# Performance work log

Measured on AMD Instinct MI355X. Metric: run time of the kernel, lower is better.

## Reference

```python
import jax, jax.numpy as jnp
import numpy as np

DEPTH, HEADS, DIM_HEAD = 6, 8, 32
D_MODEL, D_FF = 256, 1024
B, N, D_IN, N_CLS = 4, 4096, 128, 10
NB_FEAT = int(DIM_HEAD * np.log(DIM_HEAD))  # 110 random features (performer_pytorch default)


def _ortho_gaussian(m, d, rng):
    # gaussian orthogonal random projection (FAVOR+), rows rescaled by chi-distributed norms
    blocks = []
    for _ in range(int(np.ceil(m / d))):
        q, _ = np.linalg.qr(rng.standard_normal((d, d)))
        blocks.append(q.T)
    mat = np.concatenate(blocks, 0)[:m]
    mult = np.linalg.norm(rng.standard_normal((m, d)), axis=1)
    return (mult[:, None] * mat).astype(np.float32)


def setup_inputs() -> dict:
    rng = np.random.default_rng(0)
    w = lambda *s: jnp.asarray((rng.standard_normal(s) * 0.02).astype(np.float32))
    z = lambda *s: jnp.zeros(s, jnp.float32)
    o = lambda *s: jnp.ones(s, jnp.float32)
    proj = jnp.asarray(np.stack([_ortho_gaussian(NB_FEAT, DIM_HEAD, rng) for _ in range(DEPTH)]))
    return dict(
        x=jnp.asarray(rng.standard_normal((B, N, D_IN)).astype(np.float32)),
        mask=jnp.ones((B, N), bool),
        w_in=w(D_IN, D_MODEL), b_in=z(D_MODEL),
        ln1_g=o(DEPTH, D_MODEL), ln1_b=z(DEPTH, D_MODEL),
        wq=w(DEPTH, D_MODEL, D_MODEL), wk=w(DEPTH, D_MODEL, D_MODEL),
        wv=w(DEPTH, D_MODEL, D_MODEL), wo=w(DEPTH, D_MODEL, D_MODEL), bo=z(DEPTH, D_MODEL),
        proj=proj,
        ln2_g=o(DEPTH, D_MODEL), ln2_b=z(DEPTH, D_MODEL),
        w1=w(DEPTH, D_MODEL, D_FF), b1=z(DEPTH, D_FF),
        w2=w(DEPTH, D_FF, D_MODEL), b2=z(DEPTH, D_MODEL),
        cls_g=o(D_MODEL), cls_b=z(D_MODEL),
        wc1=w(D_MODEL, D_MODEL), bc1=z(D_MODEL),
        wc2=w(D_MODEL, N_CLS), bc2=z(N_CLS),
    )


def _ln(x, g, b, eps=1e-5):
    mu = x.mean(-1, keepdims=True)
    var = ((x - mu) ** 2).mean(-1, keepdims=True)
    return (x - mu) * jax.lax.rsqrt(var + eps) * g + b


def _softmax_kernel(data, proj, is_query, eps=1e-4):
    # FAVOR+ positive softmax features (performer_pytorch softmax_kernel)
    dn = data.shape[-1] ** -0.25
    ratio = proj.shape[0] ** -0.5
    dd = jnp.einsum('bhnd,md->bhnm', data * dn, proj)
    diag = 0.5 * (dn ** 2) * jnp.sum(data ** 2, axis=-1, keepdims=True)  # [B,H,N,1]
    if is_query:
        m = jnp.max(dd, axis=-1, keepdims=True)
    else:
        m = jnp.max(dd, axis=(-2, -1), keepdims=True)
    m = jax.lax.stop_gradient(m)
    return ratio * (jnp.exp(dd - diag - m) + eps)


def _linear_attn(q, k, v):
    # non-causal O(n) attention: q,k [B,H,N,M], v [B,H,N,dh]
    k_sum = k.sum(-2)                                            # [B,H,M]
    d_inv = 1.0 / jnp.einsum('bhnm,bhm->bhn', q, k_sum)          # [B,H,N]
    ctx = jnp.einsum('bhnm,bhnd->bhmd', k, v)                    # [B,H,M,dh]
    return jnp.einsum('bhnm,bhmd,bhn->bhnd', q, ctx, d_inv)


def _forward(x, mask, w_in, b_in, ln1_g, ln1_b, wq, wk, wv, wo, bo, proj,
             ln2_g, ln2_b, w1, b1, w2, b2, cls_g, cls_b, wc1, bc1, wc2, bc2):
    b_, n_ = x.shape[:2]
    h = x @ w_in + b_in
    mb = mask[:, None, :, None]
    split = lambda t: t.reshape(b_, n_, HEADS, DIM_HEAD).transpose(0, 2, 1, 3)
    for i in range(DEPTH):
        y = _ln(h, ln1_g[i], ln1_b[i])
        q, k, v = split(y @ wq[i]), split(y @ wk[i]), split(y @ wv[i])
        v = jnp.where(mb, v, 0.0)
        qp = _softmax_kernel(q, proj[i], True)
        kp = _softmax_kernel(k, proj[i], False)
        a = _linear_attn(qp, kp, v).transpose(0, 2, 1, 3).reshape(b_, n_, D_MODEL)
        h = h + a @ wo[i] + bo[i]
        y2 = _ln(h, ln2_g[i], ln2_b[i])
        h = h + jax.nn.gelu(y2 @ w1[i] + b1[i], approximate=False) @ w2[i] + b2[i]
    p = h.mean(1)
    z = jax.nn.relu(_ln(p, cls_g, cls_b))
    z = jax.nn.relu(z @ wc1 + bc1)
    return z @ wc2 + bc2


def reference(x, mask, w_in, b_in, ln1_g, ln1_b, wq, wk, wv, wo, bo, proj,
              ln2_g, ln2_b, w1, b1, w2, b2, cls_g, cls_b, wc1, bc1, wc2, bc2):
    return _forward(x, mask, w_in, b_in, ln1_g, ln1_b, wq, wk, wv, wo, bo, proj,
                    ln2_g, ln2_b, w1, b1, w2, b2, cls_g, cls_b, wc1, bc1, wc2, bc2)
```

## Files before the change

### kernel.cpp

```cpp
#include <hip/hip_runtime.h>
#include <cstdint>
#include <cstddef>

typedef __attribute__((ext_vector_type(8))) short bf16x8;
typedef __attribute__((ext_vector_type(4))) float f32x4;
typedef unsigned short u16;
typedef unsigned int u32;

static constexpr float DN    = 0.42044820762685725f;
static constexpr float DN2   = 0.17677669529663687f;
static constexpr float RATIO = 0.09534625892455924f;
static constexpr float KEPS  = 1e-4f;

__device__ __forceinline__ float b2f(u16 u) {
    union { float f; u32 i; } x; x.i = ((u32)u) << 16; return x.f;
}
__device__ __forceinline__ u16 f2b(float f) {
    union { float f; u32 i; } x; x.f = f;
    u32 r = (x.i + 0x7FFFu + ((x.i >> 16) & 1u)) >> 16;
    return (u16)r;
}
__device__ __forceinline__ float wred_sum(float v) {
#pragma unroll
    for (int o = 32; o > 0; o >>= 1) v += __shfl_xor(v, o, 64);
    return v;
}
__device__ __forceinline__ float gelu_f(float v) {
    return 0.5f * v * (1.f + erff(v * 0.7071067811865475f));
}
__device__ __forceinline__ void gload16(const u16* g, u16* l) {
    __builtin_amdgcn_global_load_lds(
        (const __attribute__((address_space(1))) u32*)(const u32*)g,
        (__attribute__((address_space(3))) u32*)(u32*)l, 16, 0, 0);
}

__global__ __launch_bounds__(256) void trk(const float* __restrict__ src, u16* __restrict__ dst,
                                           int K, int N)
{
    const size_t bo = (size_t)blockIdx.z * K * N;
    src += bo; dst += bo;
    __shared__ float tl[32][33];
    const int t = threadIdx.x, tx = t & 31, ty = t >> 5;
    const int k0 = blockIdx.y * 32, n0 = blockIdx.x * 32;
#pragma unroll
    for (int p = 0; p < 4; ++p)
        tl[ty + p * 8][tx] = src[(size_t)(k0 + ty + p * 8) * N + n0 + tx];
    __syncthreads();
#pragma unroll
    for (int p = 0; p < 4; ++p)
        dst[(size_t)(n0 + ty + p * 8) * K + k0 + tx] = f2b(tl[tx][ty + p * 8]);
}

__global__ __launch_bounds__(256) void trkf(const float* __restrict__ src, float* __restrict__ dst,
                                            int K, int N)
{
    __shared__ float tl[32][33];
    const int t = threadIdx.x, tx = t & 31, ty = t >> 5;
    const int k0 = blockIdx.y * 32, n0 = blockIdx.x * 32;
#pragma unroll
    for (int p = 0; p < 4; ++p)
        tl[ty + p * 8][tx] = src[(size_t)(k0 + ty + p * 8) * N + n0 + tx];
    __syncthreads();
#pragma unroll
    for (int p = 0; p < 4; ++p)
        dst[(size_t)(n0 + ty + p * 8) * K + k0 + tx] = tl[tx][ty + p * 8];
}

__global__ __launch_bounds__(256) void xcast(const float* __restrict__ x, u16* __restrict__ xb)
{
    const int i = blockIdx.x * 256 + threadIdx.x;
    const float4 v = ((const float4*)x)[i];
    uint2 r;
    r.x = (u32)f2b(v.x) | ((u32)f2b(v.y) << 16);
    r.y = (u32)f2b(v.z) | ((u32)f2b(v.w) << 16);
    ((uint2*)xb)[i] = r;
}

template<int CMODE, int NP, bool QKV, bool AHEAD, bool CHEAD, bool CHUNK, int DEPTH>
__global__ __launch_bounds__(512) void gemm3(
    const u16* __restrict__ A, const u16* __restrict__ Bt,
    const float* __restrict__ bias, u16* __restrict__ Cb, int ldc,
    u16* __restrict__ hres, const float* __restrict__ lng, const float* __restrict__ lnb,
    u16* __restrict__ yout, int K, int lda, int nrt)
{
    constexpr int KC    = (NP == 128) ? 256 : 128;
    constexpr int SLOTS = KC / 8;
    constexpr int SSH   = (SLOTS == 32) ? 5 : 4;
    constexpr int BB    = NP * KC * 2;
    constexpr int ABYT  = 64 * KC * 2;
    constexpr int NCB   = NP / 128;
    constexpr int CTS   = (NP == 128) ? 136 : 264;
    constexpr int EPI   = (CMODE <= 1) ? (64 * CTS * 2) : (64 * 264 * 2 + 4608);
    constexpr int KCC   = 64;
    constexpr int BBC   = 256 * KCC * 2;
    constexpr int ABYTC = 64 * KCC * 2;
    constexpr int BUF   = BBC + ABYTC;
    constexpr int LDSZ  = CHUNK ? (DEPTH * BUF) : (BB + 2 * ABYT + EPI);
    __shared__ __align__(16) char smem[LDSZ];

    const u16* Btl = Bt;
    u16* Cbl = Cb;
    if (QKV) { Btl += (size_t)blockIdx.z * 393216; Cbl += (size_t)blockIdx.z * 4194304; }
    const int t = threadIdx.x, w = t >> 6, lr = (t & 63) & 15, lg = (t & 63) >> 4;
    const int p = blockIdx.x;

    char* epi = CHUNK ? smem : (smem + BB + 2 * ABYT);

    f32x4 acc[4][NCB];
    auto ZERO = [&]() {
#pragma unroll
        for (int i = 0; i < 4; ++i)
#pragma unroll
            for (int j = 0; j < NCB; ++j) acc[i][j] = f32x4{0.f, 0.f, 0.f, 0.f};
    };

    auto EPILOGUE = [&](int row0) {
        if constexpr (CMODE <= 1) {
            u16* ctile = (u16*)epi;
            float bv[NCB];
#pragma unroll
            for (int cb = 0; cb < NCB; ++cb) {
                const int col = p * NP + w * (NP / 8) + cb * 16 + lr;
                bv[cb] = bias ? bias[col] : 0.f;
            }
#pragma unroll
            for (int rbk = 0; rbk < 4; ++rbk)
#pragma unroll
                for (int cb = 0; cb < NCB; ++cb)
#pragma unroll
                    for (int rr = 0; rr < 4; ++rr) {
                        const int rl = rbk * 16 + 4 * lg + rr;
                        float v = acc[rbk][cb][rr] + bv[cb];
                        if (CMODE == 1) v = gelu_f(v);
                        ctile[rl * CTS + w * (NP / 8) + cb * 16 + lr] = f2b(v);
                    }
            __syncthreads();
            if constexpr (CHEAD && NP == 128) {
                const int bq = row0 >> 12, n0 = row0 & 4095;
#pragma unroll
                for (int i = 0; i < 2; ++i) {
                    const int u = i * 512 + t;
                    const int hh = u >> 8, rem = u & 255;
                    const int row = rem >> 2, dblk = rem & 3;
                    *(uint4*)(Cbl + ((size_t)(bq * 8 + p * 4 + hh) * 4096 + n0 + row) * 32 + dblk * 8)
                        = *(const uint4*)&ctile[row * CTS + hh * 32 + dblk * 8];
                }
            } else if constexpr (CHEAD && NP == 256) {
                const int bq = row0 >> 12, n0 = row0 & 4095;
#pragma unroll
                for (int i = 0; i < 4; ++i) {
                    const int u = i * 512 + t;
                    const int row = u >> 5, seg = u & 31;
                    const int hh = seg >> 2, dblk = seg & 3;
                    *(uint4*)(Cbl + ((size_t)(bq * 8 + hh) * 4096 + n0 + row) * 32 + dblk * 8)
                        = *(const uint4*)&ctile[row * 264 + seg * 8];
                }
            } else {
                constexpr int NIT = (NP == 128) ? 2 : 4;
                constexpr int SEGM = NP / 8 - 1;
                constexpr int RSH = (NP == 128) ? 4 : 5;
#pragma unroll
                for (int i = 0; i < NIT; ++i) {
                    const int u = i * 512 + t;
                    const int row = u >> RSH, seg = u & SEGM;
                    *(uint4*)(Cbl + (size_t)(row0 + row) * ldc + p * NP + seg * 8)
                        = *(const uint4*)&ctile[row * CTS + seg * 8];
                }
            }
        } else {
            u16*   ctile = (u16*)epi;
            float* rsum  = (float*)(epi + 33792);
            float* rsum2 = rsum + 512;
            float* rmu   = rsum2 + 512;
            float* rrs   = rmu + 64;
            int cidx[NCB]; float bv[NCB];
#pragma unroll
            for (int cb = 0; cb < NCB; ++cb) {
                cidx[cb] = w * 32 + cb * 16 + lr;
                bv[cb] = bias ? bias[cidx[cb]] : 0.f;
            }
            if constexpr (CMODE == 2 || CMODE == 4) {
#pragma unroll
                for (int i = 0; i < 4; ++i) {
                    const int u = i * 512 + t;
                    const int row = u >> 5, seg = u & 31;
                    *(uint4*)&ctile[row * 264 + seg * 8]
                        = *(const uint4*)(hres + (size_t)(row0 + row) * 256 + seg * 8);
                }
                __syncthreads();
            }
#pragma unroll
            for (int rbk = 0; rbk < 4; ++rbk)
#pragma unroll
                for (int cb = 0; cb < NCB; ++cb)
#pragma unroll
                    for (int rr = 0; rr < 4; ++rr) {
                        const int rl = rbk * 16 + 4 * lg + rr;
                        float v = acc[rbk][cb][rr] + bv[cb];
                        if constexpr (CMODE == 2 || CMODE == 4)
                            v += b2f(ctile[rl * 264 + cidx[cb]]);
                        acc[rbk][cb][rr] = v;
                    }
            __syncthreads();
            if constexpr (CMODE != 4) {
#pragma unroll
                for (int rbk = 0; rbk < 4; ++rbk)
#pragma unroll
                    for (int rr = 0; rr < 4; ++rr) {
                        float s1 = acc[rbk][0][rr] + acc[rbk][NCB - 1][rr];
                        float s2 = fmaf(acc[rbk][0][rr], acc[rbk][0][rr],
                                        acc[rbk][NCB - 1][rr] * acc[rbk][NCB - 1][rr]);
#pragma unroll
                        for (int off = 1; off < 16; off <<= 1) {
                            s1 += __shfl_xor(s1, off, 64);
                            s2 += __shfl_xor(s2, off, 64);
                        }
                        if (lr == 0) {
                            const int rl = rbk * 16 + 4 * lg + rr;
                            rsum[rl * 8 + w] = s1; rsum2[rl * 8 + w] = s2;
                        }
                    }
                __syncthreads();
                if (t < 64) {
                    float s1 = 0.f, s2 = 0.f;
#pragma unroll
                    for (int j = 0; j < 8; ++j) { s1 += rsum[t * 8 + j]; s2 += rsum2[t * 8 + j]; }
                    const float mu = s1 * (1.f / 256.f);
                    const float var = s2 * (1.f / 256.f) - mu * mu;
                    rmu[t] = mu; rrs[t] = rsqrtf(var + 1e-5f);
                }
                __syncthreads();
            }
#pragma unroll
            for (int rbk = 0; rbk < 4; ++rbk)
#pragma unroll
                for (int cb = 0; cb < NCB; ++cb)
#pragma unroll
                    for (int rr = 0; rr < 4; ++rr) {
                        const int rl = rbk * 16 + 4 * lg + rr;
                        ctile[rl * 264 + cidx[cb]] = f2b(acc[rbk][cb][rr]);
                    }
            __syncthreads();
#pragma unroll
            for (int i = 0; i < 4; ++i) {
                const int u = i * 512 + t;
                const int row = u >> 5, seg = u & 31;
                *(uint4*)(hres + (size_t)(row0 + row) * 256 + seg * 8)
                    = *(const uint4*)&ctile[row * 264 + seg * 8];
            }
            if constexpr (CMODE != 4) {
                __syncthreads();
                float gv[NCB], bb2[NCB];
#pragma unroll
                for (int cb = 0; cb < NCB; ++cb) { gv[cb] = lng[cidx[cb]]; bb2[cb] = lnb[cidx[cb]]; }
#pragma unroll
                for (int rbk = 0; rbk < 4; ++rbk)
#pragma unroll
                    for (int cb = 0; cb < NCB; ++cb)
#pragma unroll
                        for (int rr = 0; rr < 4; ++rr) {
                            const int rl = rbk * 16 + 4 * lg + rr;
                            const float yv = (acc[rbk][cb][rr] - rmu[rl]) * rrs[rl] * gv[cb] + bb2[cb];
                            ctile[rl * 264 + cidx[cb]] = f2b(yv);
                        }
                __syncthreads();
#pragma unroll
                for (int i = 0; i < 4; ++i) {
                    const int u = i * 512 + t;
                    const int row = u >> 5, seg = u & 31;
                    *(uint4*)(yout + (size_t)(row0 + row) * 256 + seg * 8)
                        = *(const uint4*)&ctile[row * 264 + seg * 8];
                }
            }
        }
    };

    if constexpr (!CHUNK) {
        u16* Bs  = (u16*)smem;
        u16* Asm = (u16*)(smem + BB);
        auto STAGE_B = [&](int c) {
#pragma unroll
            for (int i = 0; i < BB / 16 / 512; ++i) {
                const int u = i * 512 + t;
                const int col = u >> SSH, slot = u & (SLOTS - 1);
                const int gs = slot ^ (col & 7);
                gload16(Btl + (size_t)(p * NP + col) * K + c * KC + gs * 8, Bs + u * 8);
            }
        };
        auto STAGE_A = [&](int c, int row0, int buf) {
            u16* dst = Asm + buf * (ABYT / 2);
#pragma unroll
            for (int i = 0; i < ABYT / 16 / 512; ++i) {
                const int u = i * 512 + t;
                const int row = u >> SSH, slot = u & (SLOTS - 1);
                const int gs = slot ^ (row & 7);
                const u16* src;
                if (AHEAD) {
                    const int kg = c * KC + gs * 8;
                    src = A + ((size_t)((row0 >> 12) * 8 + (kg >> 5)) * 4096 + (row0 & 4095) + row) * 32 + (kg & 31);
                } else {
                    src = A + (size_t)(row0 + row) * lda + c * KC + gs * 8;
                }
                gload16(src, dst + u * 8);
            }
        };
        auto KLOOP = [&](const u16* AcC) {
#pragma unroll
            for (int ks = 0; ks < KC / 32; ++ks) {
                bf16x8 af[4], bfv[NCB];
#pragma unroll
                for (int rbk = 0; rbk < 4; ++rbk) {
                    const int row = rbk * 16 + lr;
                    af[rbk] = *(const bf16x8*)&AcC[row * KC + (((ks * 4 + lg) ^ (row & 7)) << 3)];
                }
#pragma unroll
                for (int cb = 0; cb < NCB; ++cb) {
                    const int col = w * (NP / 8) + cb * 16 + lr;
                    bfv[cb] = *(const bf16x8*)&Bs[col * KC + (((ks * 4 + lg) ^ (col & 7)) << 3)];
                }
#pragma unroll
                for (int rbk = 0; rbk < 4; ++rbk)
#pragma unroll
                    for (int cb = 0; cb < NCB; ++cb)
                        acc[rbk][cb] = __builtin_amdgcn_mfma_f32_16x16x32_bf16(af[rbk], bfv[cb], acc[rbk][cb], 0, 0, 0);
            }
        };
        int ab = 0;
        STAGE_B(0);
        STAGE_A(0, blockIdx.y * nrt * 64, 0);
        asm volatile("s_waitcnt vmcnt(0)" ::: "memory");
        __syncthreads();
        for (int rt = 0; rt < nrt; ++rt) {
            const int row0 = (blockIdx.y * nrt + rt) * 64;
            if (rt + 1 < nrt) STAGE_A(0, row0 + 64, ab ^ 1);
            ZERO();
            KLOOP(Asm + ab * (ABYT / 2));
            EPILOGUE(row0);
            asm volatile("s_waitcnt vmcnt(0)" ::: "memory");
            __syncthreads();
            ab ^= 1;
        }
    } else {
        const int NC = K / KCC;
        const int row0 = blockIdx.y * 64;
        auto STAGE_CH = [&](int c, int b) {
            u16* bsB = (u16*)(smem + b * BUF);
            u16* bsA = (u16*)(smem + b * BUF + BBC);
#pragma unroll
            for (int i = 0; i < BBC / 16 / 512; ++i) {
                const int u = i * 512 + t;
                const int col = u >> 3, slot = u & 7;
                const int gs = slot ^ (col & 7);
                gload16(Btl + (size_t)(p * NP + col) * K + c * KCC + gs * 8, bsB + u * 8);
            }
            {
                const int u = t;
                const int row = u >> 3, slot = u & 7;
                const int gs = slot ^ (row & 7);
                const u16* src;
                if (AHEAD) {
                    const int kg = c * KCC + gs * 8;
                    src = A + ((size_t)((row0 >> 12) * 8 + (kg >> 5)) * 4096 + (row0 & 4095) + row) * 32 + (kg & 31);
                } else {
                    src = A + (size_t)(row0 + row) * lda + c * KCC + gs * 8;
                }
                gload16(src, bsA + u * 8);
            }
        };
        auto KLOOP_C = [&](const u16* BsC, const u16* AcC) {
#pragma unroll
            for (int ks = 0; ks < 2; ++ks) {
                bf16x8 af[4], bfv[NCB];
#pragma unroll
                for (int rbk = 0; rbk < 4; ++rbk) {
                    const int row = rbk * 16 + lr;
                    af[rbk] = *(const bf16x8*)&AcC[row * KCC + (((ks * 4 + lg) ^ (row & 7)) << 3)];
                }
#pragma unroll
                for (int cb = 0; cb < NCB; ++cb) {
                    const int col = w * 32 + cb * 16 + lr;
                    bfv[cb] = *(const bf16x8*)&BsC[col * KCC + (((ks * 4 + lg) ^ (col & 7)) << 3)];
                }
#pragma unroll
                for (int rbk = 0; rbk < 4; ++rbk)
#pragma unroll
                    for (int cb = 0; cb < NCB; ++cb)
                        acc[rbk][cb] = __builtin_amdgcn_mfma_f32_16x16x32_bf16(af[rbk], bfv[cb], acc[rbk][cb], 0, 0, 0);
            }
        };

        ZERO();
#pragma unroll
        for (int d = 0; d < DEPTH; ++d)
            if (d < NC) STAGE_CH(d, d);
        for (int c = 0; c < NC; ++c) {
            const int rem = NC - 1 - c;
            if constexpr (DEPTH == 3) {
                if (rem >= 2)      asm volatile("s_waitcnt vmcnt(10)" ::: "memory");
                else if (rem == 1) asm volatile("s_waitcnt vmcnt(5)"  ::: "memory");
                else               asm volatile("s_waitcnt vmcnt(0)"  ::: "memory");
            } else {
                if (rem >= 1)      asm volatile("s_waitcnt vmcnt(5)"  ::: "memory");
                else               asm volatile("s_waitcnt vmcnt(0)"  ::: "memory");
            }
            __builtin_amdgcn_s_barrier();
            __builtin_amdgcn_sched_barrier(0);
            const int cb_ = c % DEPTH;
            KLOOP_C((const u16*)(smem + cb_ * BUF),
                    (const u16*)(smem + cb_ * BUF + BBC));
            __builtin_amdgcn_sched_barrier(0);
            if (c + DEPTH < NC) {
                __builtin_amdgcn_s_barrier();
                __builtin_amdgcn_sched_barrier(0);
                STAGE_CH(c + DEPTH, cb_);
            }
        }
        __builtin_amdgcn_s_barrier();
        __builtin_amdgcn_sched_barrier(0);
        EPILOGUE(row0);
    }
}

__global__ __launch_bounds__(256) void kctx2(
    const u16* __restrict__ kg, const u16* __restrict__ vg,
    const float* __restrict__ proj, float* __restrict__ ctxp, float* __restrict__ Mcp,
    float* __restrict__ vsump)
{
    __shared__ __align__(16) u16 projS[112 * 32];
    __shared__ __align__(16) u16 kS[128 * 32];
    __shared__ __align__(16) u16 vTS[48 * 128];
    __shared__ __align__(16) u16 eTS[112 * 128];
    __shared__ float diagS[128];
    __shared__ float redS[4];
    const int t = threadIdx.x, w = t >> 6, lane = t & 63, lr = lane & 15, lg = lane >> 4;
    const int bh = blockIdx.x >> 3, chunk = blockIdx.x & 7;

    for (int idx = t; idx < 112 * 32; idx += 256) {
        const int m = idx >> 5, d = idx & 31;
        projS[idx] = (m < 110) ? f2b(proj[m * 32 + d] * DN) : (u16)0;
    }
    for (int idx = t; idx < 16 * 128; idx += 256) {
        const int rr = idx >> 7;
        vTS[(32 + rr) * 128 + (idx & 127)] = (rr == 0) ? f2b(1.0f) : (u16)0;
    }
    for (int idx = t; idx < 16 * 128; idx += 256)
        eTS[112 * 128 + idx] = 0;

    f32x4 E[2][3];
#pragma unroll
    for (int i = 0; i < 2; ++i)
#pragma unroll
        for (int j = 0; j < 3; ++j) E[i][j] = f32x4{0.f, 0.f, 0.f, 0.f};
    float Mrun = -INFINITY;
    float vsAcc = 0.f;

    for (int r = 0; r < 4; ++r) {
        const size_t eb = ((size_t)bh * 4096 + chunk * 512 + r * 128) * 32;
#pragma unroll
        for (int i = 0; i < 2; ++i) {
            const int u = i * 256 + t;
            ((uint4*)kS)[u] = ((const uint4*)(kg + eb))[u];
        }
#pragma unroll
        for (int i = 0; i < 2; ++i) {
            const int u = i * 256 + t;
            const int tok = u >> 2, dblk = u & 3;
            union { uint4 v; u16 s[8]; } uu;
            uu.v = ((const uint4*)(vg + eb))[u];
#pragma unroll
            for (int j = 0; j < 8; ++j) {
                const int d = dblk * 8 + j;
                vTS[d * 128 + ((((tok >> 3) ^ (d & 15))) << 3) + (tok & 7)] = uu.s[j];
            }
        }
        __syncthreads();
        {
            const int d = t >> 3, seg = t & 7;
            union { uint4 v; u16 s[8]; } ua, ub;
            ua.v = *(const uint4*)&vTS[d * 128 + seg * 16];
            ub.v = *(const uint4*)&vTS[d * 128 + seg * 16 + 8];
            float s = 0.f;
#pragma unroll
            for (int j = 0; j < 8; ++j) s += b2f(ua.s[j]) + b2f(ub.s[j]);
            vsAcc += s;
        }
        if (t < 128) {
            float s = 0.f;
#pragma unroll
            for (int dq = 0; dq < 4; ++dq) {
                union { uint4 v; u16 ss[8]; } uu;
                uu.v = ((const uint4*)kS)[t * 4 + dq];
#pragma unroll
                for (int j = 0; j < 8; ++j) { const float f = b2f(uu.ss[j]); s = fmaf(f, f, s); }
            }
            diagS[t] = 0.5f * DN2 * s;
        }
        __syncthreads();
        f32x4 dd[7][2];
#pragma unroll
        for (int mb = 0; mb < 7; ++mb)
#pragma unroll
            for (int tb = 0; tb < 2; ++tb) dd[mb][tb] = f32x4{0.f, 0.f, 0.f, 0.f};
        bf16x8 kf[2];
#pragma unroll
        for (int tb = 0; tb < 2; ++tb)
            kf[tb] = *(const bf16x8*)&kS[(w * 32 + tb * 16 + lr) * 32 + lg * 8];
#pragma unroll
        for (int mb = 0; mb < 7; ++mb) {
            const bf16x8 pf = *(const bf16x8*)&projS[(mb * 16 + lr) * 32 + lg * 8];
#pragma unroll
            for (int tb = 0; tb < 2; ++tb)
                dd[mb][tb] = __builtin_amdgcn_mfma_f32_16x16x32_bf16(pf, kf[tb], dd[mb][tb], 0, 0, 0);
        }
        float mx = -INFINITY;
#pragma unroll
        for (int mb = 0; mb < 7; ++mb)
#pragma unroll
            for (int tb = 0; tb < 2; ++tb)
#pragma unroll
                for (int rr = 0; rr < 4; ++rr) {
                    if (mb == 6 && (4 * lg + rr) >= 14) continue;
                    mx = fmaxf(mx, dd[mb][tb][rr]);
                }
#pragma unroll
        for (int off = 1; off < 64; off <<= 1) mx = fmaxf(mx, __shfl_xor(mx, off, 64));
        if (lane == 0) redS[w] = mx;
        __syncthreads();
        float Mnew = fmaxf(fmaxf(redS[0], redS[1]), fmaxf(redS[2], redS[3]));
        Mnew = fmaxf(Mrun, Mnew);
        const float scl = __expf(Mrun - Mnew);
#pragma unroll
        for (int i = 0; i < 2; ++i)
#pragma unroll
            for (int j = 0; j < 3; ++j)
#pragma unroll
                for (int rr = 0; rr < 4; ++rr) E[i][j][rr] *= scl;
        Mrun = Mnew;
        const float dg0 = diagS[w * 32 + lr], dg1 = diagS[w * 32 + 16 + lr];
#pragma unroll
        for (int mb = 0; mb < 7; ++mb)
#pragma unroll
            for (int tb = 0; tb < 2; ++tb)
#pragma unroll
                for (int rr = 0; rr < 4; ++rr) {
                    const int tok = w * 32 + tb * 16 + lr;
                    const int m = mb * 16 + 4 * lg + rr;
                    const float e = __expf(dd[mb][tb][rr] - (tb ? dg1 : dg0) - Mnew);
                    eTS[m * 128 + ((((tok >> 3) ^ (m & 15))) << 3) + (tok & 7)] = f2b(e);
                }
        __syncthreads();
#pragma unroll
        for (int ks = 0; ks < 4; ++ks) {
            bf16x8 aF[2], bF[3];
#pragma unroll
            for (int mb2 = 0; mb2 < 2; ++mb2) {
                const int m = w * 32 + mb2 * 16 + lr;
                aF[mb2] = *(const bf16x8*)&eTS[m * 128 + (((ks * 4 + lg) ^ lr) << 3)];
            }
#pragma unroll
            for (int nb = 0; nb < 3; ++nb) {
                const int d = nb * 16 + lr;
                bF[nb] = *(const bf16x8*)&vTS[d * 128 + (((ks * 4 + lg) ^ lr) << 3)];
            }
#pragma unroll
            for (int mb2 = 0; mb2 < 2; ++mb2)
#pragma unroll
                for (int nb = 0; nb < 3; ++nb)
                    E[mb2][nb] = __builtin_amdgcn_mfma_f32_16x16x32_bf16(aF[mb2], bF[nb], E[mb2][nb], 0, 0, 0);
        }
        __syncthreads();
    }
    const size_t ob = (size_t)blockIdx.x * 112 * 33;
// ... 162 lines not shown
    f32x4 o[2][2];
#pragma unroll
    for (int i = 0; i < 2; ++i)
#pragma unroll
        for (int j = 0; j < 2; ++j) o[i][j] = f32x4{0.f, 0.f, 0.f, 0.f};
#pragma unroll
    for (int ks = 0; ks < 4; ++ks) {
        bf16x8 aF[2], bF[2];
#pragma unroll
        for (int tb = 0; tb < 2; ++tb) {
            const int tok = w * 32 + tb * 16 + lr;
            aF[tb] = *(const bf16x8*)&pS[tok * 128 + (((ks * 4 + lg) ^ lr) << 3)];
        }
#pragma unroll
        for (int nb = 0; nb < 2; ++nb) {
            const int d = nb * 16 + lr;
            bF[nb] = *(const bf16x8*)&ctxTS[d * 128 + (((ks * 4 + lg) ^ lr) << 3)];
        }
#pragma unroll
        for (int tb = 0; tb < 2; ++tb)
#pragma unroll
            for (int nb = 0; nb < 2; ++nb)
                o[tb][nb] = __builtin_amdgcn_mfma_f32_16x16x32_bf16(aF[tb], bF[nb], o[tb][nb], 0, 0, 0);
    }
    u16* outS = qS;
#pragma unroll
    for (int tb = 0; tb < 2; ++tb)
#pragma unroll
        for (int nb = 0; nb < 2; ++nb)
#pragma unroll
            for (int rr = 0; rr < 4; ++rr) {
                const int tokl = w * 32 + tb * 16 + 4 * lg + rr;
                outS[tokl * 32 + nb * 16 + lr] = f2b(o[tb][nb][rr] * dinvS[tokl]);
            }
    __syncthreads();
#pragma unroll
    for (int i = 0; i < 2; ++i) {
        const int u = i * 256 + t;
        ((uint4*)(ag + qeb))[u] = ((const uint4*)outS)[u];
    }
}

__global__ __launch_bounds__(256) void pool_k(const u16* __restrict__ h,
                                              float* __restrict__ pp)
{
    const int b = blockIdx.x, ch = blockIdx.y, d = threadIdx.x;
    const u16* p = h + ((size_t)b * 4096 + ch * 256) * 256 + d;
    float s = 0.f;
    for (int n = 0; n < 256; ++n) s += b2f(p[(size_t)n * 256]);
    pp[(b * 16 + ch) * 256 + d] = s;
}

__global__ __launch_bounds__(256) void cls_a(const float* __restrict__ pp,
                                             const float* __restrict__ g,
                                             const float* __restrict__ bb,
                                             float* __restrict__ zA)
{
    const int b = blockIdx.x, t = threadIdx.x, w = t >> 6, lane = t & 63;
    __shared__ float red1[4], red2[4];
    float s = 0.f;
#pragma unroll
    for (int c = 0; c < 16; ++c) s += pp[(b * 16 + c) * 256 + t];
    const float p = s * (1.f / 4096.f);
    const float s1 = wred_sum(p);
    const float s2 = wred_sum(p * p);
    if (lane == 0) { red1[w] = s1; red2[w] = s2; }
    __syncthreads();
    const float S1 = red1[0] + red1[1] + red1[2] + red1[3];
    const float S2 = red2[0] + red2[1] + red2[2] + red2[3];
    const float mu = S1 * (1.f / 256.f);
    const float var = S2 * (1.f / 256.f) - mu * mu;
    const float rr = rsqrtf(var + 1e-5f);
    zA[b * 256 + t] = fmaxf((p - mu) * rr * g[t] + bb[t], 0.f);
}

__global__ __launch_bounds__(256) void cls_b(const float* __restrict__ zA,
                                             const float* __restrict__ wc1T,
                                             const float* __restrict__ bc1,
                                             float* __restrict__ zB)
{
    const int b = blockIdx.x, t = threadIdx.x;
    __shared__ float zS[256];
    zS[t] = zA[b * 256 + t];
    __syncthreads();
    float s = bc1[t];
    const float* wr = wc1T + (size_t)t * 256;
#pragma unroll
    for (int i = 0; i < 64; ++i) {
        const float4 v = ((const float4*)wr)[i];
        s = fmaf(zS[i * 4 + 0], v.x, s);
        s = fmaf(zS[i * 4 + 1], v.y, s);
        s = fmaf(zS[i * 4 + 2], v.z, s);
        s = fmaf(zS[i * 4 + 3], v.w, s);
    }
    zB[b * 256 + t] = fmaxf(s, 0.f);
}

__global__ __launch_bounds__(256) void cls_c(const float* __restrict__ zB,
                                             const float* __restrict__ wc2,
                                             const float* __restrict__ bc2,
                                             float* __restrict__ out)
{
    const int b = blockIdx.x, t = threadIdx.x, w = t >> 6, lane = t & 63;
    __shared__ float red[4][10];
    const float v = zB[b * 256 + t];
    float a[10];
#pragma unroll
    for (int c = 0; c < 10; ++c) a[c] = v * wc2[t * 10 + c];
#pragma unroll
    for (int c = 0; c < 10; ++c) {
        const float s = wred_sum(a[c]);
        if (lane == 0) red[w][c] = s;
    }
    __syncthreads();
    if (t < 10) out[b * 10 + t] = bc2[t] + red[0][t] + red[1][t] + red[2][t] + red[3][t];
}

extern "C" void kernel_launch(void* const* d_in, const int* in_sizes, int n_in,
                              void* d_out, int out_size, void* d_ws, size_t ws_size,
                              hipStream_t stream)
{
    const float* x    = (const float*)d_in[0];
    const float* w_in = (const float*)d_in[2];
    const float* b_in = (const float*)d_in[3];
    const float* ln1g = (const float*)d_in[4];
    const float* ln1b = (const float*)d_in[5];
    const float* wq   = (const float*)d_in[6];
    const float* wk   = (const float*)d_in[7];
    const float* wv   = (const float*)d_in[8];
    const float* wo   = (const float*)d_in[9];
    const float* bo   = (const float*)d_in[10];
    const float* proj = (const float*)d_in[11];
    const float* ln2g = (const float*)d_in[12];
    const float* ln2b = (const float*)d_in[13];
    const float* w1   = (const float*)d_in[14];
    const float* b1   = (const float*)d_in[15];
    const float* w2   = (const float*)d_in[16];
    const float* b2   = (const float*)d_in[17];
    const float* clsg = (const float*)d_in[18];
    const float* clsb = (const float*)d_in[19];
    const float* wc1  = (const float*)d_in[20];
    const float* bc1  = (const float*)d_in[21];
    const float* wc2  = (const float*)d_in[22];
    const float* bc2  = (const float*)d_in[23];

    char* wsb = (char*)d_ws;
    const size_t MB = 1024 * 1024;
    u16* h     = (u16*)(wsb);
    u16* y     = (u16*)(wsb + 16 * MB);
    u16* qb    = (u16*)(wsb + 24 * MB);
    u16* kb    = (u16*)(wsb + 32 * MB);
    u16* vb    = (u16*)(wsb + 40 * MB);
    u16* ab    = (u16*)(wsb + 48 * MB);
    u16* mid   = qb;
    u16* xb    = (u16*)(wsb + 56 * MB);
    u16* wtb   = (u16*)(wsb + 60 * MB);
    u16* w_inT = wtb;
    u16* wqT   = w_inT + 32768;
    u16* wkT   = wqT + 393216;
    u16* wvT   = wkT + 393216;
    u16* woT   = wvT + 393216;
    u16* w1T   = woT + 393216;
    u16* w2T   = w1T + 1572864;
    char* p2   = (char*)(w2T + 1572864);
    float* ctxp  = (float*)p2;
    float* Mcp   = ctxp + 256 * 112 * 33;
    u16*   ctxTg = (u16*)(Mcp + 256);
    float* ksumg = (float*)(ctxTg + 32 * 4096);
    float* pp    = ksumg + 32 * 128;
    float* vsump = pp + 16384;
    float* zA    = vsump + 8192;
    float* zB    = zA + 1024;
    float* wc1T  = zB + 1024;

    trk<<<dim3(8, 4, 1), 256, 0, stream>>>(w_in, w_inT, 128, 256);
    trk<<<dim3(8, 8, 6), 256, 0, stream>>>(wq, wqT, 256, 256);
    trk<<<dim3(8, 8, 6), 256, 0, stream>>>(wk, wkT, 256, 256);
    trk<<<dim3(8, 8, 6), 256, 0, stream>>>(wv, wvT, 256, 256);
    trk<<<dim3(8, 8, 6), 256, 0, stream>>>(wo, woT, 256, 256);
    trk<<<dim3(32, 8, 6), 256, 0, stream>>>(w1, w1T, 256, 1024);
    trk<<<dim3(8, 32, 6), 256, 0, stream>>>(w2, w2T, 1024, 256);
    trkf<<<dim3(8, 8, 1), 256, 0, stream>>>(wc1, wc1T, 256, 256);
    xcast<<<2048, 256, 0, stream>>>(x, xb);

    gemm3<3, 256, false, false, false, false, 2><<<dim3(1, 256), 512, 0, stream>>>(
        xb, w_inT, b_in, nullptr, 256, h, ln1g, ln1b, y, 128, 128, 1);
    for (int i = 0; i < 6; ++i) {
        const float* proj_i = proj + (size_t)i * 3520;
        gemm3<0, 256, true, false, true, true, 2><<<dim3(1, 256, 3), 512, 0, stream>>>(
            y, wqT + (size_t)i * 65536, nullptr, qb, 256,
            nullptr, nullptr, nullptr, nullptr, 256, 256, 1);
        kctx2<<<256, 256, 0, stream>>>(kb, vb, proj_i, ctxp, Mcp, vsump);
        kred2<<<32, 256, 0, stream>>>(ctxp, Mcp, vsump, ctxTg, ksumg);
        qattn2<<<1024, 256, 0, stream>>>(qb, proj_i, ctxTg, ksumg, ab);
        gemm3<2, 256, false, true, false, true, 3><<<dim3(1, 256), 512, 0, stream>>>(
            ab, woT + (size_t)i * 65536, bo + i * 256, nullptr, 256, h,
            ln2g + i * 256, ln2b + i * 256, y, 256, 0, 1);
        gemm3<1, 256, false, false, false, true, 2><<<dim3(4, 256), 512, 0, stream>>>(
            y, w1T + (size_t)i * 262144, b1 + i * 1024, mid, 1024,
            nullptr, nullptr, nullptr, nullptr, 256, 256, 1);
        if (i < 5)
            gemm3<2, 256, false, false, false, true, 3><<<dim3(1, 256), 512, 0, stream>>>(
                mid, w2T + (size_t)i * 262144, b2 + i * 256, nullptr, 256, h,
                ln1g + (i + 1) * 256, ln1b + (i + 1) * 256, y, 1024, 1024, 1);
        else
            gemm3<4, 256, false, false, false, true, 3><<<dim3(1, 256), 512, 0, stream>>>(
                mid, w2T + (size_t)i * 262144, b2 + i * 256, nullptr, 256, h,
                nullptr, nullptr, nullptr, 1024, 1024, 1);
    }
    pool_k<<<dim3(4, 16), 256, 0, stream>>>(h, pp);
    cls_a<<<4, 256, 0, stream>>>(pp, clsg, clsb, zA);
    cls_b<<<4, 256, 0, stream>>>(zA, wc1T, bc1, zB);
    cls_c<<<4, 256, 0, stream>>>(zB, wc2, bc2, (float*)d_out);
}
```

Baseline: 821.4 us.

## Fuse FFN up-projection, GELU and down-projection into one kernel

Replaces the separate W1 GEMM (writing a 1024-wide intermediate to global memory) and W2 GEMM with a single kernel per 64-row tile. The kernel computes 256-column chunks of the GELU intermediate into shared memory and immediately accumulates them into the W2 output, then applies bias, residual and the next LayerNorm. This removes the global write and read of the intermediate activation and one launch per layer. In exchange it uses 128KB of shared memory per block with only 256 blocks, which lowers occupancy and parallelism, and it reads y and writes y in place, which is safe only because each block stages its own rows first.

```diff
diff --git a/kernel.cpp b/kernel.cpp
--- a/kernel.cpp
+++ b/kernel.cpp
@@ -418,6 +418,238 @@
         __builtin_amdgcn_s_barrier();
         __builtin_amdgcn_sched_barrier(0);
         EPILOGUE(row0);
+    }
+}
+
+template<int CMODE2>
+__global__ __launch_bounds__(512) void ffuse(
+    const u16* __restrict__ yg, const u16* __restrict__ w1T, const float* __restrict__ b1,
+    const u16* __restrict__ w2T, const float* __restrict__ b2,
+    u16* __restrict__ hres, const float* __restrict__ lng, const float* __restrict__ lnb,
+    u16* __restrict__ yout)
+{
+    __shared__ __align__(16) char smem[131072];
+    u16* yS   = (u16*)smem;
+    u16* midS = (u16*)(smem + 32768);
+    u16* wb   = (u16*)(smem + 65536);
+    char* epi = smem + 65536;
+
+    const int t = threadIdx.x, w = t >> 6, lr = (t & 63) & 15, lg = (t & 63) >> 4;
+    const int row0 = blockIdx.x * 64;
+
+#pragma unroll
+    for (int i = 0; i < 4; ++i) {
+        const int u = i * 512 + t;
+        const int row = u >> 5, s32 = u & 31;
+        const int kc = s32 >> 3, sl = s32 & 7;
+        const int gs = sl ^ (row & 7);
+        gload16(yg + (size_t)(row0 + row) * 256 + kc * 64 + gs * 8, yS + u * 8);
+    }
+
+    auto STAGE_J = [&](int j, int b) {
+        const int mp = j >> 3, ph = (j >> 2) & 1, kc = j & 3;
+        u16* dst = wb + b * 16384;
+#pragma unroll
+        for (int i = 0; i < 4; ++i) {
+            const int u = i * 512 + t;
+            const int col = u >> 3, sl = u & 7;
+            const int gs = sl ^ (col & 7);
+            const u16* src = (ph == 0)
+                ? (w1T + (size_t)(mp * 256 + col) * 256 + kc * 64 + gs * 8)
+                : (w2T + (size_t)col * 1024 + mp * 256 + kc * 64 + gs * 8);
+            gload16(src, dst + u * 8);
+        }
+    };
+
+    f32x4 acc1[4][2], acc2[4][2];
+#pragma unroll
+    for (int i = 0; i < 4; ++i)
+#pragma unroll
+        for (int j = 0; j < 2; ++j) acc2[i][j] = f32x4{0.f, 0.f, 0.f, 0.f};
+
+    STAGE_J(0, 0);
+    STAGE_J(1, 1);
+
+#pragma unroll
+    for (int j = 0; j < 32; ++j) {
+        if (j < 31) asm volatile("s_waitcnt vmcnt(4)" ::: "memory");
+        else        asm volatile("s_waitcnt vmcnt(0)" ::: "memory");
+        __builtin_amdgcn_s_barrier();
+        __builtin_amdgcn_sched_barrier(0);
+        const int mp = j >> 3, ph = (j >> 2) & 1, kc = j & 3;
+        const u16* wc = wb + (j & 1) * 16384;
+        if (ph == 0) {
+            if (kc == 0) {
+#pragma unroll
+                for (int i = 0; i < 4; ++i)
+#pragma unroll
+                    for (int jj = 0; jj < 2; ++jj) acc1[i][jj] = f32x4{0.f, 0.f, 0.f, 0.f};
+            }
+#pragma unroll
+            for (int ks = 0; ks < 2; ++ks) {
+                bf16x8 af[4], bfv[2];
+#pragma unroll
+                for (int rbk = 0; rbk < 4; ++rbk) {
+                    const int row = rbk * 16 + lr;
+                    af[rbk] = *(const bf16x8*)&yS[row * 256 + kc * 64 + (((ks * 4 + lg) ^ (row & 7)) << 3)];
+                }
+#pragma unroll
+                for (int cb = 0; cb < 2; ++cb) {
+                    const int col = w * 32 + cb * 16 + lr;
+                    bfv[cb] = *(const bf16x8*)&wc[col * 64 + (((ks * 4 + lg) ^ (col & 7)) << 3)];
+                }
+#pragma unroll
+                for (int rbk = 0; rbk < 4; ++rbk)
+#pragma unroll
+                    for (int cb = 0; cb < 2; ++cb)
+                        acc1[rbk][cb] = __builtin_amdgcn_mfma_f32_16x16x32_bf16(af[rbk], bfv[cb], acc1[rbk][cb], 0, 0, 0);
+            }
+        } else {
+#pragma unroll
+            for (int ks = 0; ks < 2; ++ks) {
+                bf16x8 af[4], bfv[2];
+#pragma unroll
+                for (int rbk = 0; rbk < 4; ++rbk) {
+                    const int row = rbk * 16 + lr;
+                    af[rbk] = *(const bf16x8*)&midS[row * 256 + kc * 64 + (((ks * 4 + lg) ^ (row & 7)) << 3)];
+                }
+#pragma unroll
+                for (int cb = 0; cb < 2; ++cb) {
+                    const int col = w * 32 + cb * 16 + lr;
+                    bfv[cb] = *(const bf16x8*)&wc[col * 64 + (((ks * 4 + lg) ^ (col & 7)) << 3)];
+                }
+#pragma unroll
+                for (int rbk = 0; rbk < 4; ++rbk)
+#pragma unroll
+                    for (int cb = 0; cb < 2; ++cb)
+                        acc2[rbk][cb] = __builtin_amdgcn_mfma_f32_16x16x32_bf16(af[rbk], bfv[cb], acc2[rbk][cb], 0, 0, 0);
+            }
+        }
+        __builtin_amdgcn_sched_barrier(0);
+        if (ph == 0 && kc == 3) {
+#pragma unroll
+            for (int rbk = 0; rbk < 4; ++rbk)
+#pragma unroll
+                for (int cb = 0; cb < 2; ++cb) {
+                    const int col = w * 32 + cb * 16 + lr;
+                    const float bv = b1[mp * 256 + col];
+#pragma unroll
+                    for (int rr = 0; rr < 4; ++rr) {
+                        const int row = rbk * 16 + 4 * lg + rr;
+                        const float v = gelu_f(acc1[rbk][cb][rr] + bv);
+                        midS[row * 256 + (col & ~63) + ((((col >> 3) & 7) ^ (row & 7)) << 3) + (col & 7)] = f2b(v);
+                    }
+                }
+            asm volatile("s_waitcnt lgkmcnt(0)" ::: "memory");
+            __builtin_amdgcn_sched_barrier(0);
+        }
+        if (j + 2 < 32) {
+            __builtin_amdgcn_s_barrier();
+            __builtin_amdgcn_sched_barrier(0);
+            STAGE_J(j + 2, j & 1);
+        }
+    }
+    __builtin_amdgcn_s_barrier();
+    __builtin_amdgcn_sched_barrier(0);
+
+    u16*   ctile = (u16*)epi;
+    float* rsum  = (float*)(epi + 33792);
+    float* rsum2 = rsum + 512;
+    float* rmu   = rsum2 + 512;
+    float* rrs   = rmu + 64;
+    int cidx[2]; float bv[2];
+#pragma unroll
+    for (int cb = 0; cb < 2; ++cb) {
+        cidx[cb] = w * 32 + cb * 16 + lr;
+        bv[cb] = b2[cidx[cb]];
+    }
+#pragma unroll
+    for (int i = 0; i < 4; ++i) {
+        const int u = i * 512 + t;
+        const int row = u >> 5, seg = u & 31;
+        *(uint4*)&ctile[row * 264 + seg * 8]
+            = *(const uint4*)(hres + (size_t)(row0 + row) * 256 + seg * 8);
+    }
+    __syncthreads();
+#pragma unroll
+    for (int rbk = 0; rbk < 4; ++rbk)
+#pragma unroll
+        for (int cb = 0; cb < 2; ++cb)
+#pragma unroll
+            for (int rr = 0; rr < 4; ++rr) {
+                const int rl = rbk * 16 + 4 * lg + rr;
+                acc2[rbk][cb][rr] += bv[cb] + b2f(ctile[rl * 264 + cidx[cb]]);
+            }
+    __syncthreads();
+    if constexpr (CMODE2 != 4) {
+#pragma unroll
+        for (int rbk = 0; rbk < 4; ++rbk)
+#pragma unroll
+            for (int rr = 0; rr < 4; ++rr) {
+                float s1 = acc2[rbk][0][rr] + acc2[rbk][1][rr];
+                float s2 = fmaf(acc2[rbk][0][rr], acc2[rbk][0][rr],
+                                acc2[rbk][1][rr] * acc2[rbk][1][rr]);
+#pragma unroll
+                for (int off = 1; off < 16; off <<= 1) {
+                    s1 += __shfl_xor(s1, off, 64);
+                    s2 += __shfl_xor(s2, off, 64);
+                }
+                if (lr == 0) {
+                    const int rl = rbk * 16 + 4 * lg + rr;
+                    rsum[rl * 8 + w] = s1; rsum2[rl * 8 + w] = s2;
+                }
+            }
+        __syncthreads();
+        if (t < 64) {
+            float s1 = 0.f, s2 = 0.f;
+#pragma unroll
+            for (int jj = 0; jj < 8; ++jj) { s1 += rsum[t * 8 + jj]; s2 += rsum2[t * 8 + jj]; }
+            const float mu = s1 * (1.f / 256.f);
+            const float var = s2 * (1.f / 256.f) - mu * mu;
+            rmu[t] = mu; rrs[t] = rsqrtf(var + 1e-5f);
+        }
+        __syncthreads();
+    }
+#pragma unroll
+    for (int rbk = 0; rbk < 4; ++rbk)
+#pragma unroll
+        for (int cb = 0; cb < 2; ++cb)
+#pragma unroll
+            for (int rr = 0; rr < 4; ++rr) {
+                const int rl = rbk * 16 + 4 * lg + rr;
+                ctile[rl * 264 + cidx[cb]] = f2b(acc2[rbk][cb][rr]);
+            }
+    __syncthreads();
+#pragma unroll
+    for (int i = 0; i < 4; ++i) {
+        const int u = i * 512 + t;
+        const int row = u >> 5, seg = u & 31;
+        *(uint4*)(hres + (size_t)(row0 + row) * 256 + seg * 8)
+            = *(const uint4*)&ctile[row * 264 + seg * 8];
+    }
+    if constexpr (CMODE2 != 4) {
+        __syncthreads();
+        float gv[2], bb2[2];
+#pragma unroll
+        for (int cb = 0; cb < 2; ++cb) { gv[cb] = lng[cidx[cb]]; bb2[cb] = lnb[cidx[cb]]; }
+#pragma unroll
+        for (int rbk = 0; rbk < 4; ++rbk)
+#pragma unroll
+            for (int cb = 0; cb < 2; ++cb)
+#pragma unroll
+                for (int rr = 0; rr < 4; ++rr) {
+                    const int rl = rbk * 16 + 4 * lg + rr;
+                    const float yv = (acc2[rbk][cb][rr] - rmu[rl]) * rrs[rl] * gv[cb] + bb2[cb];
+                    ctile[rl * 264 + cidx[cb]] = f2b(yv);
+                }
+        __syncthreads();
+#pragma unroll
+        for (int i = 0; i < 4; ++i) {
+            const int u = i * 512 + t;
+            const int row = u >> 5, seg = u & 31;
+            *(uint4*)(yout + (size_t)(row0 + row) * 256 + seg * 8)
+                = *(const uint4*)&ctile[row * 264 + seg * 8];
+        }
     }
 }
 
@@ -886,7 +1118,6 @@
     u16* kb    = (u16*)(wsb + 32 * MB);
     u16* vb    = (u16*)(wsb + 40 * MB);
     u16* ab    = (u16*)(wsb + 48 * MB);
-    u16* mid   = qb;
     u16* xb    = (u16*)(wsb + 56 * MB);
     u16* wtb   = (u16*)(wsb + 60 * MB);
     u16* w_inT = wtb;
@@ -930,17 +1161,16 @@
         gemm3<2, 256, false, true, false, true, 3><<<dim3(1, 256), 512, 0, stream>>>(
             ab, woT + (size_t)i * 65536, bo + i * 256, nullptr, 256, h,
             ln2g + i * 256, ln2b + i * 256, y, 256, 0, 1);
-        gemm3<1, 256, false, false, false, true, 2><<<dim3(4, 256), 512, 0, stream>>>(
-            y, w1T + (size_t)i * 262144, b1 + i * 1024, mid, 1024,
-            nullptr, nullptr, nullptr, nullptr, 256, 256, 1);
         if (i < 5)
-            gemm3<2, 256, false, false, false, true, 3><<<dim3(1, 256), 512, 0, stream>>>(
-                mid, w2T + (size_t)i * 262144, b2 + i * 256, nullptr, 256, h,
-                ln1g + (i + 1) * 256, ln1b + (i + 1) * 256, y, 1024, 1024, 1);
+            ffuse<2><<<256, 512, 0, stream>>>(
+                y, w1T + (size_t)i * 262144, b1 + i * 1024,
+                w2T + (size_t)i * 262144, b2 + i * 256,
+                h, ln1g + (i + 1) * 256, ln1b + (i + 1) * 256, y);
         else
-            gemm3<4, 256, false, false, false, true, 3><<<dim3(1, 256), 512, 0, stream>>>(
-                mid, w2T + (size_t)i * 262144, b2 + i * 256, nullptr, 256, h,
-                nullptr, nullptr, nullptr, 1024, 1024, 1);
+            ffuse<4><<<256, 512, 0, stream>>>(
+                y, w1T + (size_t)i * 262144, b1 + i * 1024,
+                w2T + (size_t)i * 262144, b2 + i * 256,
+                h, nullptr, nullptr, y);
     }
     pool_k<<<dim3(4, 16), 256, 0, stream>>>(h, pp);
     cls_a<<<4, 256, 0, stream>>>(pp, clsg, clsb, zA);
```

Result: no change. 827.0 us (+0.7%).

## Split residual GEMMs into 128-column tiles and move LayerNorm to separate kernel

Applied to the files above, without the earlier changes.

The out-projection and FFN-down GEMMs previously used one 256-column block per 64-row tile and fused residual add plus LayerNorm in the epilogue. They now use 128-column tiles (twice as many blocks) with a residual-add-only epilogue, followed by a standalone LayerNorm kernel. The chunked pipeline is also fixed at double buffering. This raises block-level parallelism for the 256-wide GEMMs, at the cost of an extra read and write of h per LayerNorm and more kernel launches.

```diff
diff --git a/kernel.cpp b/kernel.cpp
--- a/kernel.cpp
+++ b/kernel.cpp
@@ -76,6 +76,31 @@
     ((uint2*)xb)[i] = r;
 }
 
+__global__ __launch_bounds__(256) void lnk(const u16* __restrict__ h,
+                                           const float* __restrict__ g,
+                                           const float* __restrict__ bb,
+                                           u16* __restrict__ y)
+{
+    const int row = blockIdx.x * 4 + (threadIdx.x >> 6);
+    const int lane = threadIdx.x & 63;
+    const uint2 v = *(const uint2*)(h + (size_t)row * 256 + lane * 4);
+    float f[4];
+    f[0] = b2f((u16)(v.x & 0xFFFF)); f[1] = b2f((u16)(v.x >> 16));
+    f[2] = b2f((u16)(v.y & 0xFFFF)); f[3] = b2f((u16)(v.y >> 16));
+    float s = f[0] + f[1] + f[2] + f[3];
+    float ss = fmaf(f[0], f[0], fmaf(f[1], f[1], fmaf(f[2], f[2], f[3] * f[3])));
+    s = wred_sum(s); ss = wred_sum(ss);
+    const float mu = s * (1.f / 256.f);
+    const float var = ss * (1.f / 256.f) - mu * mu;
+    const float rr = rsqrtf(var + 1e-5f);
+    const float4 gv = *(const float4*)(g + lane * 4);
+    const float4 bv = *(const float4*)(bb + lane * 4);
+    uint2 o;
+    o.x = (u32)f2b((f[0] - mu) * rr * gv.x + bv.x) | ((u32)f2b((f[1] - mu) * rr * gv.y + bv.y) << 16);
+    o.y = (u32)f2b((f[2] - mu) * rr * gv.z + bv.z) | ((u32)f2b((f[3] - mu) * rr * gv.w + bv.w) << 16);
+    *(uint2*)(y + (size_t)row * 256 + lane * 4) = o;
+}
+
 template<int CMODE, int NP, bool QKV, bool AHEAD, bool CHEAD, bool CHUNK, int DEPTH>
 __global__ __launch_bounds__(512) void gemm3(
     const u16* __restrict__ A, const u16* __restrict__ Bt,
@@ -83,16 +108,16 @@
     u16* __restrict__ hres, const float* __restrict__ lng, const float* __restrict__ lnb,
     u16* __restrict__ yout, int K, int lda, int nrt)
 {
-    constexpr int KC    = (NP == 128) ? 256 : 128;
+    constexpr int KC    = 128;
     constexpr int SLOTS = KC / 8;
-    constexpr int SSH   = (SLOTS == 32) ? 5 : 4;
+    constexpr int SSH   = 4;
     constexpr int BB    = NP * KC * 2;
     constexpr int ABYT  = 64 * KC * 2;
     constexpr int NCB   = NP / 128;
     constexpr int CTS   = (NP == 128) ? 136 : 264;
     constexpr int EPI   = (CMODE <= 1) ? (64 * CTS * 2) : (64 * 264 * 2 + 4608);
     constexpr int KCC   = 64;
-    constexpr int BBC   = 256 * KCC * 2;
+    constexpr int BBC   = NP * KCC * 2;
     constexpr int ABYTC = 64 * KCC * 2;
     constexpr int BUF   = BBC + ABYTC;
     constexpr int LDSZ  = CHUNK ? (DEPTH * BUF) : (BB + 2 * ABYT + EPI);
@@ -135,17 +160,7 @@
                         ctile[rl * CTS + w * (NP / 8) + cb * 16 + lr] = f2b(v);
                     }
             __syncthreads();
-            if constexpr (CHEAD && NP == 128) {
-                const int bq = row0 >> 12, n0 = row0 & 4095;
-#pragma unroll
-                for (int i = 0; i < 2; ++i) {
-                    const int u = i * 512 + t;
-                    const int hh = u >> 8, rem = u & 255;
-                    const int row = rem >> 2, dblk = rem & 3;
-                    *(uint4*)(Cbl + ((size_t)(bq * 8 + p * 4 + hh) * 4096 + n0 + row) * 32 + dblk * 8)
-                        = *(const uint4*)&ctile[row * CTS + hh * 32 + dblk * 8];
-                }
-            } else if constexpr (CHEAD && NP == 256) {
+            if constexpr (CHEAD && NP == 256) {
                 const int bq = row0 >> 12, n0 = row0 & 4095;
 #pragma unroll
                 for (int i = 0; i < 4; ++i) {
@@ -166,6 +181,34 @@
                     *(uint4*)(Cbl + (size_t)(row0 + row) * ldc + p * NP + seg * 8)
                         = *(const uint4*)&ctile[row * CTS + seg * 8];
                 }
+            }
+        } else if constexpr (NP == 128) {
+            u16* ctile = (u16*)epi;
+            const int cidx = w * 16 + lr;
+            const float bv = bias ? bias[p * 128 + cidx] : 0.f;
+#pragma unroll
+            for (int i = 0; i < 2; ++i) {
+                const int u = i * 512 + t;
+                const int row = u >> 4, seg = u & 15;
+                *(uint4*)&ctile[row * 136 + seg * 8]
+                    = *(const uint4*)(hres + (size_t)(row0 + row) * 256 + p * 128 + seg * 8);
+            }
+            __syncthreads();
+#pragma unroll
+            for (int rbk = 0; rbk < 4; ++rbk)
+#pragma unroll
+                for (int rr = 0; rr < 4; ++rr) {
+                    const int rl = rbk * 16 + 4 * lg + rr;
+                    const float v = acc[rbk][0][rr] + bv + b2f(ctile[rl * 136 + cidx]);
+                    ctile[rl * 136 + cidx] = f2b(v);
+                }
+            __syncthreads();
+#pragma unroll
+            for (int i = 0; i < 2; ++i) {
+                const int u = i * 512 + t;
+                const int row = u >> 4, seg = u & 15;
+                *(uint4*)(hres + (size_t)(row0 + row) * 256 + p * 128 + seg * 8)
+                    = *(const uint4*)&ctile[row * 136 + seg * 8];
             }
         } else {
             u16*   ctile = (u16*)epi;
@@ -294,14 +337,7 @@
                 const int u = i * 512 + t;
                 const int row = u >> SSH, slot = u & (SLOTS - 1);
                 const int gs = slot ^ (row & 7);
-                const u16* src;
-                if (AHEAD) {
-                    const int kg = c * KC + gs * 8;
-                    src = A + ((size_t)((row0 >> 12) * 8 + (kg >> 5)) * 4096 + (row0 & 4095) + row) * 32 + (kg & 31);
-                } else {
-                    src = A + (size_t)(row0 + row) * lda + c * KC + gs * 8;
-                }
-                gload16(src, dst + u * 8);
+                gload16(A + (size_t)(row0 + row) * lda + c * KC + gs * 8, dst + u * 8);
             }
         };
         auto KLOOP = [&](const u16* AcC) {
@@ -378,7 +414,7 @@
                 }
 #pragma unroll
                 for (int cb = 0; cb < NCB; ++cb) {
-                    const int col = w * 32 + cb * 16 + lr;
+                    const int col = w * (NP / 8) + cb * 16 + lr;
                     bfv[cb] = *(const bf16x8*)&BsC[col * KCC + (((ks * 4 + lg) ^ (col & 7)) << 3)];
                 }
 #pragma unroll
@@ -390,29 +426,26 @@
         };
 
         ZERO();
-#pragma unroll
-        for (int d = 0; d < DEPTH; ++d)
-            if (d < NC) STAGE_CH(d, d);
+        STAGE_CH(0, 0);
+        if (1 < NC) STAGE_CH(1, 1);
         for (int c = 0; c < NC; ++c) {
             const int rem = NC - 1 - c;
-            if constexpr (DEPTH == 3) {
-                if (rem >= 2)      asm volatile("s_waitcnt vmcnt(10)" ::: "memory");
-                else if (rem == 1) asm volatile("s_waitcnt vmcnt(5)"  ::: "memory");
-                else               asm volatile("s_waitcnt vmcnt(0)"  ::: "memory");
+            if (rem >= 1) {
+                if constexpr (NP == 256) asm volatile("s_waitcnt vmcnt(5)" ::: "memory");
+                else                     asm volatile("s_waitcnt vmcnt(3)" ::: "memory");
             } else {
-                if (rem >= 1)      asm volatile("s_waitcnt vmcnt(5)"  ::: "memory");
-                else               asm volatile("s_waitcnt vmcnt(0)"  ::: "memory");
+                asm volatile("s_waitcnt vmcnt(0)" ::: "memory");
             }
             __builtin_amdgcn_s_barrier();
             __builtin_amdgcn_sched_barrier(0);
-            const int cb_ = c % DEPTH;
+            const int cb_ = c & 1;
             KLOOP_C((const u16*)(smem + cb_ * BUF),
                     (const u16*)(smem + cb_ * BUF + BBC));
             __builtin_amdgcn_sched_barrier(0);
-            if (c + DEPTH < NC) {
+            if (c + 2 < NC) {
                 __builtin_amdgcn_s_barrier();
                 __builtin_amdgcn_sched_barrier(0);
-                STAGE_CH(c + DEPTH, cb_);
+                STAGE_CH(c + 2, cb_);
             }
         }
         __builtin_amdgcn_s_barrier();
@@ -927,20 +960,18 @@
         kctx2<<<256, 256, 0, stream>>>(kb, vb, proj_i, ctxp, Mcp, vsump);
         kred2<<<32, 256, 0, stream>>>(ctxp, Mcp, vsump, ctxTg, ksumg);
         qattn2<<<1024, 256, 0, stream>>>(qb, proj_i, ctxTg, ksumg, ab);
-        gemm3<2, 256, false, true, false, true, 3><<<dim3(1, 256), 512, 0, stream>>>(
+        gemm3<4, 128, false, true, false, true, 2><<<dim3(2, 256), 512, 0, stream>>>(
             ab, woT + (size_t)i * 65536, bo + i * 256, nullptr, 256, h,
-            ln2g + i * 256, ln2b + i * 256, y, 256, 0, 1);
+            nullptr, nullptr, nullptr, 256, 0, 1);
+        lnk<<<4096, 256, 0, stream>>>(h, ln2g + i * 256, ln2b + i * 256, y);
         gemm3<1, 256, false, false, false, true, 2><<<dim3(4, 256), 512, 0, stream>>>(
             y, w1T + (size_t)i * 262144, b1 + i * 1024, mid, 1024,
             nullptr, nullptr, nullptr, nullptr, 256, 256, 1);
+        gemm3<4, 128, false, false, false, true, 2><<<dim3(2, 256), 512, 0, stream>>>(
+            mid, w2T + (size_t)i * 262144, b2 + i * 256, nullptr, 256, h,
+            nullptr, nullptr, nullptr, 1024, 1024, 1);
         if (i < 5)
-            gemm3<2, 256, false, false, false, true, 3><<<dim3(1, 256), 512, 0, stream>>>(
-                mid, w2T + (size_t)i * 262144, b2 + i * 256, nullptr, 256, h,
-                ln1g + (i + 1) * 256, ln1b + (i + 1) * 256, y, 1024, 1024, 1);
-        else
-            gemm3<4, 256, false, false, false, true, 3><<<dim3(1, 256), 512, 0, stream>>>(
-                mid, w2T + (size_t)i * 262144, b2 + i * 256, nullptr, 256, h,
-                nullptr, nullptr, nullptr, 1024, 1024, 1);
+            lnk<<<4096, 256, 0, stream>>>(h, ln1g + (i + 1) * 256, ln1b + (i + 1) * 256, y);
     }
     pool_k<<<dim3(4, 16), 256, 0, stream>>>(h, pp);
     cls_a<<<4, 256, 0, stream>>>(pp, clsg, clsb, zA);
```

Measured after the change: 779.3 us. -5.1%, faster.
